# Kernel optimization log

Hardware: AMD Instinct MI355X
Metric: run time of the kernel (lower is better)

The kernel has to match this reference:

```python
import jax, jax.numpy as jnp
import numpy as np

T = 128          # number_of_trees
B = 1024         # batch_size
D = 28 * 28      # hardcoded feature dim
K = 200          # hardcoded top-k


def setup_inputs() -> dict:
    key = jax.random.key(0)
    k1, k2 = jax.random.split(key)
    x = jax.random.normal(k1, (B, D), dtype=jnp.float32)
    attention_mask = jax.random.uniform(k2, (T, D), dtype=jnp.float32, minval=-1.0, maxval=1.0)
    return {"x": x, "attention_mask": attention_mask}


def reference(x, attention_mask):
    # sigmoid -> top-k -> scatter builds a sparse per-tree mask [T, D]
    att = jax.nn.sigmoid(attention_mask)                      # [T, D]
    topk, idx = jax.lax.top_k(att, K)                         # [T, K] each
    rows = jnp.arange(T)[:, None]                             # [T, 1]
    attention = jnp.zeros((T, D), dtype=att.dtype).at[rows, idx].set(topk)  # [T, D]
    # per-tree broadcast multiply, vectorized (replaces python loop over trees)
    xf = x.reshape(-1, D)                                     # [B, D]
    return_value = xf[:, None, :] * attention[None, :, :]     # [B, T, D]
    return (return_value, attention)
```

## Files before the change

### kernel.cpp

```cpp
#include <hip/hip_runtime.h>
#include <math.h>

#define NT 128
#define NB 1024
#define ND 784
#define NK 200
#define ND4 196

__global__ __launch_bounds__(256) void topk_attention_kernel(
    const float* __restrict__ mask, float* __restrict__ att_out)
{
    __shared__ unsigned int su[ND];
    __shared__ float        sv[ND];
    __shared__ unsigned char sel[ND];
    __shared__ int          cnts[32];

    const int t   = blockIdx.x;
    const int tid = threadIdx.x;

    if (tid < 32) cnts[tid] = 0;

    for (int d = tid; d < ND; d += 256) {
        float f = mask[t * ND + d];
        unsigned int b = __float_as_uint(f);
        su[d]  = ((int)b < 0) ? ~b : (b | 0x80000000u);
        sv[d]  = 1.0f / (1.0f + expf(-f));
        sel[d] = 0;
    }
    __syncthreads();

    unsigned int p = 0;
    int need = NK;
    for (int bit = 31; bit >= 0; --bit) {
        const unsigned int test = (p | (1u << bit)) >> bit;
        int local = 0;
        for (int d = tid; d < ND; d += 256)
            local += ((su[d] >> bit) == test) ? 1 : 0;
        #pragma unroll
        for (int off = 32; off > 0; off >>= 1)
            local += __shfl_down(local, off);
        if ((tid & 63) == 0) atomicAdd(&cnts[bit], local);
        __syncthreads();
        const int c = cnts[bit];
        if (c >= need) p |= (1u << bit);
        else           need -= c;
    }

    for (int d = tid; d < ND; d += 256)
        sel[d] = (su[d] > p) ? 1 : 0;
    __syncthreads();
    if (tid == 0) {
        int rem = need;
        for (int d = 0; d < ND && rem > 0; ++d)
            if (su[d] == p) { sel[d] = 1; --rem; }
    }
    __syncthreads();

    for (int d = tid; d < ND; d += 256)
        att_out[t * ND + d] = sel[d] ? sv[d] : 0.0f;
}

__global__ __launch_bounds__(256) void bcast_mul_kernel(
    const float4* __restrict__ x4, const float4* __restrict__ att4,
    float4* __restrict__ out4)
{
    const int total4 = NB * NT * ND4;
    const int stride = gridDim.x * blockDim.x;
    for (int idx = blockIdx.x * 256 + threadIdx.x; idx < total4; idx += stride) {
        const int bt = idx / ND4;
        const int d4 = idx - bt * ND4;
        const int t  = bt & (NT - 1);
        const int b  = bt >> 7;
        const float4 xv = x4[b * ND4 + d4];
        const float4 av = att4[t * ND4 + d4];
        float4 o;
        o.x = xv.x * av.x; o.y = xv.y * av.y;
        o.z = xv.z * av.z; o.w = xv.w * av.w;
        out4[idx] = o;
    }
}

extern "C" void kernel_launch(void* const* d_in, const int* in_sizes, int n_in,
                              void* d_out, int out_size, void* d_ws, size_t ws_size,
                              hipStream_t stream)
{
    (void)in_sizes; (void)n_in; (void)out_size; (void)d_ws; (void)ws_size;
    const float* x    = (const float*)d_in[0];
    const float* mask = (const float*)d_in[1];
    float* out = (float*)d_out;
    float* att = out + (size_t)NB * NT * ND;

    topk_attention_kernel<<<NT, 256, 0, stream>>>(mask, att);

    const int total4 = NB * NT * ND4;
    const int grid   = total4 / (256 * 4);
    bcast_mul_kernel<<<grid, 256, 0, stream>>>(
        (const float4*)x, (const float4*)att, (float4*)out);
}
```

Baseline: 512.8 us.

## Assign one block per batch row, stage x in LDS, use nontemporal stores

The broadcast-multiply kernel now launches one block per batch row. Each block loads that row of x into shared memory once, then streams the whole att table while writing the [T,D] output slice with nontemporal stores. This replaces the grid-stride loop that re-read x from global memory per element and did a div/mod to decode indices. The nontemporal hint is meant to keep the huge write-once output from polluting the caches. The cost is fewer, longer blocks and an extra barrier per block.

```diff
diff --git a/kernel.cpp b/kernel.cpp
--- a/kernel.cpp
+++ b/kernel.cpp
@@ -6,6 +6,8 @@
 #define ND 784
 #define NK 200
 #define ND4 196
+
+typedef float vfloat4 __attribute__((ext_vector_type(4)));
 
 __global__ __launch_bounds__(256) void topk_attention_kernel(
     const float* __restrict__ mask, float* __restrict__ att_out)
@@ -61,22 +63,24 @@
 }
 
 __global__ __launch_bounds__(256) void bcast_mul_kernel(
-    const float4* __restrict__ x4, const float4* __restrict__ att4,
-    float4* __restrict__ out4)
+    const vfloat4* __restrict__ x4, const vfloat4* __restrict__ att4,
+    vfloat4* __restrict__ out4)
 {
-    const int total4 = NB * NT * ND4;
-    const int stride = gridDim.x * blockDim.x;
-    for (int idx = blockIdx.x * 256 + threadIdx.x; idx < total4; idx += stride) {
-        const int bt = idx / ND4;
-        const int d4 = idx - bt * ND4;
-        const int t  = bt & (NT - 1);
-        const int b  = bt >> 7;
-        const float4 xv = x4[b * ND4 + d4];
-        const float4 av = att4[t * ND4 + d4];
-        float4 o;
-        o.x = xv.x * av.x; o.y = xv.y * av.y;
-        o.z = xv.z * av.z; o.w = xv.w * av.w;
-        out4[idx] = o;
+    __shared__ vfloat4 sx[ND4];
+    const int b   = blockIdx.x;
+    const int tid = threadIdx.x;
+    if (tid < ND4) sx[tid] = x4[b * ND4 + tid];
+    __syncthreads();
+
+    vfloat4* __restrict__ outb = out4 + (size_t)b * (NT * ND4);
+    #pragma unroll 2
+    for (int i = tid; i < NT * ND4; i += 256) {
+        const int t  = i / ND4;
+        const int d4 = i - t * ND4;
+        const vfloat4 av = att4[i];
+        const vfloat4 xv = sx[d4];
+        const vfloat4 o  = xv * av;
+        __builtin_nontemporal_store(o, &outb[i]);
     }
 }
 
@@ -92,8 +96,6 @@
 
     topk_attention_kernel<<<NT, 256, 0, stream>>>(mask, att);
 
-    const int total4 = NB * NT * ND4;
-    const int grid   = total4 / (256 * 4);
-    bcast_mul_kernel<<<grid, 256, 0, stream>>>(
-        (const float4*)x, (const float4*)att, (float4*)out);
+    bcast_mul_kernel<<<NB, 256, 0, stream>>>(
+        (const vfloat4*)x, (const vfloat4*)att, (vfloat4*)out);
 }
```

New measurement: 483.7 us. 5.7% less time.
